# Kernel tuning notes

Measured on AMD Instinct MI355X. Metric: run time of the kernel, lower is better.

## Reference

```python
import jax, jax.numpy as jnp
import numpy as np

NUM_QUERIES = 300

B, S, NUM_LABELS, D = 32, 8400, 80, 256


def setup_inputs() -> dict:
    key = jax.random.key(0)
    k1, k2, k3, k4 = jax.random.split(key, 4)
    return {
        "enc_outputs_class": jax.random.normal(k1, (B, S, NUM_LABELS), dtype=jnp.float32),
        "enc_outputs_coord": jax.random.normal(k2, (B, S, 4), dtype=jnp.float32),
        "output_memory": jax.random.normal(k3, (B, S, D), dtype=jnp.float32),
        "sources_last_element": jax.random.normal(k4, (B, 400, D), dtype=jnp.float32),
    }


def reference(enc_outputs_class, enc_outputs_coord, output_memory, sources_last_element):
    # Per-token confidence: max over class logits. [B, S]
    scores = jnp.max(enc_outputs_class, axis=-1)
    # Top-k token indices per batch element (sorted=True as in keras.ops.top_k).
    _, topk_ind = jax.lax.top_k(scores, NUM_QUERIES)  # [B, K]
    idx = topk_ind[:, :, None]  # [B, K, 1], broadcasts over feature dim

    # Batched gathers (vectorized replacement for keras.ops.map + take).
    reference_points_unact = jnp.take_along_axis(enc_outputs_coord, idx, axis=1)  # [B, K, 4]
    enc_topk_logits = jnp.take_along_axis(enc_outputs_class, idx, axis=1)  # [B, K, NUM_LABELS]
    enc_topk_bboxes = jax.nn.sigmoid(reference_points_unact)  # [B, K, 4]

    # learn_initial_query=False path: gather decoder targets from encoder memory.
    target = jax.lax.stop_gradient(jnp.take_along_axis(output_memory, idx, axis=1))  # [B, K, D]

    init_reference_points = jax.lax.stop_gradient(reference_points_unact)
    return (init_reference_points, target, enc_topk_logits, enc_topk_bboxes)
```

## Files before the change

### kernel.cpp

```cpp
#include <hip/hip_runtime.h>
#include <stdint.h>

#define BB 32
#define SS 8400
#define LL 80
#define DD 256
#define KK 300

__device__ __forceinline__ uint32_t f32_desc_ord(float f) {
    uint32_t u = __builtin_bit_cast(uint32_t, f);
    uint32_t asc = (u & 0x80000000u) ? ~u : (u | 0x80000000u);
    return ~asc;
}

__global__ __launch_bounds__(256) void k_scores(const float* __restrict__ cls,
                                                uint32_t* __restrict__ keys32) {
    int r = blockIdx.x * 256 + threadIdx.x;
    const float4* row = (const float4*)(cls + (size_t)r * LL);
    float m = -3.4e38f;
#pragma unroll
    for (int i = 0; i < 20; ++i) {
        float4 v = row[i];
        m = fmaxf(m, fmaxf(fmaxf(v.x, v.y), fmaxf(v.z, v.w)));
    }
    keys32[r] = f32_desc_ord(m);
}

__global__ __launch_bounds__(256) void k_topk(const uint32_t* __restrict__ keys32,
                                              int* __restrict__ topk) {
    __shared__ unsigned long long keys[SS];
    __shared__ uint32_t hist[256];
    __shared__ unsigned long long sel[512];
    __shared__ unsigned long long sh_prefix;
    __shared__ uint32_t sh_k, sh_cnt;

    const int b = blockIdx.x;
    const int tid = threadIdx.x;
    const uint32_t* src = keys32 + (size_t)b * SS;

    for (int i = tid; i < SS; i += 256)
        keys[i] = ((unsigned long long)src[i] << 32) | (uint32_t)i;
    if (tid == 0) { sh_prefix = 0ull; sh_k = KK; sh_cnt = 0; }
    __syncthreads();

    for (int pos = 56; pos >= 0; pos -= 8) {
        hist[tid] = 0;
        __syncthreads();
        unsigned long long pref = sh_prefix;
        for (int i = tid; i < SS; i += 256) {
            unsigned long long key = keys[i];
            if (pos == 56 || (key >> (pos + 8)) == pref)
                atomicAdd(&hist[(uint32_t)(key >> pos) & 0xFFu], 1u);
        }
        __syncthreads();
        if (tid == 0) {
            uint32_t k = sh_k, cum = 0, d;
            for (d = 0; d < 256u; ++d) {
                if (cum + hist[d] >= k) break;
                cum += hist[d];
            }
            sh_k = k - cum;
            sh_prefix = (pref << 8) | d;
        }
        __syncthreads();
    }
    const unsigned long long T = sh_prefix;

    for (int i = tid; i < SS; i += 256) {
        unsigned long long key = keys[i];
        if (key <= T) {
            uint32_t p = atomicAdd(&sh_cnt, 1u);
            if (p < 512u) sel[p] = key;
        }
    }
    __syncthreads();
    uint32_t cnt = sh_cnt;
    if (cnt > 512u) cnt = 512u;
    for (int i = tid; i < 512; i += 256)
        if ((uint32_t)i >= cnt) sel[i] = ~0ull;

    for (int k2 = 2; k2 <= 512; k2 <<= 1) {
        for (int j = k2 >> 1; j > 0; j >>= 1) {
            __syncthreads();
            for (int i = tid; i < 512; i += 256) {
                int ixj = i ^ j;
                if (ixj > i) {
                    unsigned long long a = sel[i], c = sel[ixj];
                    bool asc2 = ((i & k2) == 0);
                    if ((a > c) == asc2) { sel[i] = c; sel[ixj] = a; }
                }
            }
        }
    }
    __syncthreads();
    for (int i = tid; i < KK; i += 256)
        topk[b * KK + i] = (int)(uint32_t)(sel[i] & 0xFFFFFFFFull);
}

__global__ __launch_bounds__(64) void k_gather(const float* __restrict__ coord,
                                               const float* __restrict__ cls,
                                               const float* __restrict__ mem,
                                               const int* __restrict__ topk,
                                               float* __restrict__ out) {
    const int r = blockIdx.x;
    const int b = r / KK;
    const int t = threadIdx.x;
    const int idx = topk[r];
    const size_t srow = (size_t)b * SS + (size_t)idx;

    const size_t O1 = (size_t)BB * KK * 4;
    const size_t O2 = O1 + (size_t)BB * KK * DD;
    const size_t O3 = O2 + (size_t)BB * KK * LL;

    {
        const float4* s = (const float4*)(mem + srow * DD);
        float4* d = (float4*)(out + O1 + (size_t)r * DD);
        d[t] = s[t];
    }
    if (t < 20) {
        const float4* s = (const float4*)(cls + srow * LL);
        float4* d = (float4*)(out + O2 + (size_t)r * LL);
        d[t] = s[t];
    }
    if (t == 0) {
        float4 v = *(const float4*)(coord + srow * 4);
        *(float4*)(out + (size_t)r * 4) = v;
        float4 o;
        o.x = 1.0f / (1.0f + expf(-v.x));
        o.y = 1.0f / (1.0f + expf(-v.y));
        o.z = 1.0f / (1.0f + expf(-v.z));
        o.w = 1.0f / (1.0f + expf(-v.w));
        *(float4*)(out + O3 + (size_t)r * 4) = o;
    }
}

extern "C" void kernel_launch(void* const* d_in, const int* in_sizes, int n_in,
                              void* d_out, int out_size, void* d_ws, size_t ws_size,
                              hipStream_t stream) {
    const float* cls   = (const float*)d_in[0];
    const float* coord = (const float*)d_in[1];
    const float* mem   = (const float*)d_in[2];
    float* out = (float*)d_out;

    uint32_t* keys32 = (uint32_t*)d_ws;
    int* topk = (int*)((char*)d_ws + (size_t)BB * SS * 4);

    k_scores<<<(BB * SS) / 256, 256, 0, stream>>>(cls, keys32);
    k_topk<<<BB, 256, 0, stream>>>(keys32, topk);
    k_gather<<<BB * KK, 64, 0, stream>>>(coord, cls, mem, topk, out);
}
```

Baseline: 470.9 us.

## Speed up per-batch top-k radix select with 32-bit keys and wave-aggregated histograms

The top-k kernel now keeps 32-bit score keys in shared memory instead of packed 64-bit key-and-index values. That halves the radix passes from eight to four. Each wave merges equal histogram digits through ballot-based matching, so only one atomic is issued per unique digit. The serial thread-0 digit search is replaced by a parallel wave-level prefix scan. The bitonic sort of the candidates is replaced by a rank-by-counting placement. The block also grows to 1024 threads to use more parallelism per batch. The rank step is quadratic in the candidate count, and heavy ties at the threshold could still overflow the 512-entry candidate buffer.

```diff
diff --git a/kernel.cpp b/kernel.cpp
--- a/kernel.cpp
+++ b/kernel.cpp
@@ -26,75 +26,91 @@
     keys32[r] = f32_desc_ord(m);
 }
 
-__global__ __launch_bounds__(256) void k_topk(const uint32_t* __restrict__ keys32,
-                                              int* __restrict__ topk) {
-    __shared__ unsigned long long keys[SS];
+__global__ __launch_bounds__(1024) void k_topk(const uint32_t* __restrict__ keys32,
+                                               int* __restrict__ topk) {
+    __shared__ uint32_t keys[SS];
     __shared__ uint32_t hist[256];
+    __shared__ uint32_t wsum[4];
     __shared__ unsigned long long sel[512];
-    __shared__ unsigned long long sh_prefix;
-    __shared__ uint32_t sh_k, sh_cnt;
+    __shared__ uint32_t sh_prefix, sh_k, sh_cnt;
 
     const int b = blockIdx.x;
     const int tid = threadIdx.x;
+    const int lane = tid & 63;
     const uint32_t* src = keys32 + (size_t)b * SS;
 
-    for (int i = tid; i < SS; i += 256)
-        keys[i] = ((unsigned long long)src[i] << 32) | (uint32_t)i;
-    if (tid == 0) { sh_prefix = 0ull; sh_k = KK; sh_cnt = 0; }
+    for (int i = tid; i < SS; i += 1024) keys[i] = src[i];
+    if (tid == 0) { sh_prefix = 0u; sh_k = KK; sh_cnt = 0u; }
     __syncthreads();
 
-    for (int pos = 56; pos >= 0; pos -= 8) {
-        hist[tid] = 0;
+    for (int pos = 24; pos >= 0; pos -= 8) {
+        if (tid < 256) hist[tid] = 0u;
+        const uint32_t pref = sh_prefix;
+        const uint32_t krem = sh_k;
         __syncthreads();
-        unsigned long long pref = sh_prefix;
-        for (int i = tid; i < SS; i += 256) {
-            unsigned long long key = keys[i];
-            if (pos == 56 || (key >> (pos + 8)) == pref)
-                atomicAdd(&hist[(uint32_t)(key >> pos) & 0xFFu], 1u);
+
+#pragma unroll
+        for (int r = 0; r < 9; ++r) {
+            int i = tid + r * 1024;
+            uint32_t d = 256u;
+            if (i < SS) {
+                uint32_t key = keys[i];
+                if (pos == 24 || (key >> (pos + 8)) == pref)
+                    d = (key >> pos) & 0xFFu;
+            }
+            unsigned long long mask = ~0ull;
+#pragma unroll
+            for (int bit = 0; bit < 9; ++bit) {
+                unsigned long long bb = __ballot((d >> bit) & 1u);
+                mask &= ((d >> bit) & 1u) ? bb : ~bb;
+            }
+            if (d < 256u && (int)__builtin_ctzll(mask) == lane)
+                atomicAdd(&hist[d], (uint32_t)__popcll(mask));
         }
         __syncthreads();
-        if (tid == 0) {
-            uint32_t k = sh_k, cum = 0, d;
-            for (d = 0; d < 256u; ++d) {
-                if (cum + hist[d] >= k) break;
-                cum += hist[d];
+
+        uint32_t h = 0u, cwave = 0u;
+        if (tid < 256) {
+            h = hist[tid];
+            cwave = h;
+#pragma unroll
+            for (int off = 1; off < 64; off <<= 1) {
+                uint32_t n = __shfl_up(cwave, (unsigned)off, 64);
+                if (lane >= off) cwave += n;
             }
-            sh_k = k - cum;
-            sh_prefix = (pref << 8) | d;
+            if (lane == 63) wsum[tid >> 6] = cwave;
+        }
+        __syncthreads();
+        if (tid < 256) {
+            uint32_t base = 0u;
+            for (int w = 0; w < (tid >> 6); ++w) base += wsum[w];
+            uint32_t cumInc = base + cwave;
+            uint32_t cumExc = cumInc - h;
+            if (cumExc < krem && krem <= cumInc) {
+                sh_prefix = (pref << 8) | (uint32_t)tid;
+                sh_k = krem - cumExc;
+            }
         }
         __syncthreads();
     }
-    const unsigned long long T = sh_prefix;
 
-    for (int i = tid; i < SS; i += 256) {
-        unsigned long long key = keys[i];
+    const uint32_t T = sh_prefix;
+    for (int i = tid; i < SS; i += 1024) {
+        uint32_t key = keys[i];
         if (key <= T) {
             uint32_t p = atomicAdd(&sh_cnt, 1u);
-            if (p < 512u) sel[p] = key;
+            if (p < 512u) sel[p] = ((unsigned long long)key << 32) | (uint32_t)i;
         }
     }
     __syncthreads();
-    uint32_t cnt = sh_cnt;
-    if (cnt > 512u) cnt = 512u;
-    for (int i = tid; i < 512; i += 256)
-        if ((uint32_t)i >= cnt) sel[i] = ~0ull;
 
-    for (int k2 = 2; k2 <= 512; k2 <<= 1) {
-        for (int j = k2 >> 1; j > 0; j >>= 1) {
-            __syncthreads();
-            for (int i = tid; i < 512; i += 256) {
-                int ixj = i ^ j;
-                if (ixj > i) {
-                    unsigned long long a = sel[i], c = sel[ixj];
-                    bool asc2 = ((i & k2) == 0);
-                    if ((a > c) == asc2) { sel[i] = c; sel[ixj] = a; }
-                }
-            }
-        }
+    uint32_t cnt = sh_cnt < 512u ? sh_cnt : 512u;
+    if (tid < (int)cnt) {
+        unsigned long long mine = sel[tid];
+        uint32_t rank = 0u;
+        for (uint32_t m = 0; m < cnt; ++m) rank += (sel[m] < mine) ? 1u : 0u;
+        if (rank < KK) topk[b * KK + rank] = (int)(uint32_t)(mine & 0xFFFFFFFFull);
     }
-    __syncthreads();
-    for (int i = tid; i < KK; i += 256)
-        topk[b * KK + i] = (int)(uint32_t)(sel[i] & 0xFFFFFFFFull);
 }
 
 __global__ __launch_bounds__(64) void k_gather(const float* __restrict__ coord,
@@ -146,6 +162,6 @@
     int* topk = (int*)((char*)d_ws + (size_t)BB * SS * 4);
 
     k_scores<<<(BB * SS) / 256, 256, 0, stream>>>(cls, keys32);
-    k_topk<<<BB, 256, 0, stream>>>(keys32, topk);
+    k_topk<<<BB, 1024, 0, stream>>>(keys32, topk);
     k_gather<<<BB * KK, 64, 0, stream>>>(coord, cls, mem, topk, out);
 }
```

New measurement: 408.8 us. 13.2% less time.
